# Kernel tuning notes

Measured on AMD Instinct MI355X. Metric: run time of the kernel, lower is better.

## Reference

```python
import jax, jax.numpy as jnp
import numpy as np

LAYERS = 2
N_NODE = 100000
EMB = 112
BATCH = 512
SEQ = 50
NNZ = 1600000


def setup_inputs() -> dict:
    key = jax.random.key(0)
    ks = jax.random.split(key, 12)
    embedding = jax.random.normal(ks[0], (N_NODE, EMB), jnp.float32) * 0.1
    adj_rows = jax.random.randint(ks[1], (NNZ,), 0, N_NODE, jnp.int32)
    adj_cols = jax.random.randint(ks[2], (NNZ,), 0, N_NODE, jnp.int32)
    adj_vals = jax.random.uniform(ks[3], (NNZ,), jnp.float32) * 0.05  # normalized-ish weights
    W_q = jax.random.normal(ks[4], (EMB, EMB), jnp.float32) * 0.1
    W_k = jax.random.normal(ks[5], (EMB, EMB), jnp.float32) * 0.1
    w_sess = jax.random.normal(ks[6], (LAYERS, EMB, EMB), jnp.float32) * 0.1
    D = jax.random.uniform(ks[7], (BATCH, BATCH), jnp.float32) * 0.01
    A = jax.random.uniform(ks[8], (BATCH, BATCH), jnp.float32)
    session_len = jax.random.randint(ks[9], (BATCH, 1), 1, SEQ + 1, jnp.int32)
    mask = (jnp.arange(SEQ)[None, :] < session_len).astype(jnp.float32)  # [B,L]
    raw_items = jax.random.randint(ks[10], (BATCH, SEQ), 1, N_NODE + 1, jnp.int32)
    session_item = jnp.where(mask > 0, raw_items, 0)  # 0 = padding row in cl_embed
    return {
        "embedding": embedding, "adj_vals": adj_vals, "W_q": W_q, "W_k": W_k,
        "w_sess": w_sess, "D": D, "A": A, "adj_rows": adj_rows,
        "adj_cols": adj_cols, "session_item": session_item,
        "session_len": session_len, "mask": mask,
    }


def reference(embedding, adj_vals, W_q, W_k, w_sess, D, A,
              adj_rows, adj_cols, session_item, session_len, mask):
    dt = embedding.dtype
    # ---- HyperConv: layers x sparse.mm, then mean over layer stack ----
    emb = embedding
    acc = embedding
    for _ in range(LAYERS):
        msg = adj_vals[:, None] * emb[adj_cols]              # [nnz, d]
        emb = jax.ops.segment_sum(msg, adj_rows, num_segments=N_NODE)
        acc = acc + emb
    item_emb = acc / (LAYERS + 1)                            # [N, d]

    # ---- SR_IEM sigmoid attention pooling ----
    d = jnp.asarray(EMB, dt)
    cl = jnp.concatenate([jnp.zeros((1, EMB), dt), item_emb], axis=0)
    seq = cl[session_item]                                   # [B,L,d]
    Q = jax.nn.sigmoid(jnp.einsum('bld,de->ble', seq, W_q))
    K = jax.nn.sigmoid(jnp.einsum('bld,de->ble', seq, W_k))
    C = jax.nn.sigmoid(jnp.einsum('ble,bme->blm', Q, K)) / jnp.sqrt(d)  # [B,L,L]
    C = C * (mask[:, :, None] * mask[:, None, :])
    C = C * (1.0 - jnp.eye(SEQ, dtype=dt))                   # remove diagonal
    alpha = jnp.sum(C, axis=2) / session_len.astype(dt)      # [B,L]
    # per-session softmax over the first session_len positions == masked softmax
    beta = jax.nn.softmax(jnp.where(mask > 0, alpha, -1e9), axis=1)
    seq_h = jnp.einsum('bl,bld->bd', beta, seq)              # [B,d]

    # ---- SessConv propagation over session graph ----
    DA = D @ A                                               # [B,B]
    s = seq_h
    acc2 = seq_h
    for i in range(LAYERS):
        s = s @ w_sess[i].T                                  # Linear, no bias
        s = DA @ s
        norm = jnp.maximum(jnp.linalg.norm(s, axis=-1, keepdims=True), 1e-12)
        acc2 = acc2 + s / norm                               # F.normalize(p=2)
    return acc2 / (LAYERS + 1)                               # [B,d]
```

## Files before the change

### kernel.cpp

```cpp
#include <hip/hip_runtime.h>

#define N_NODE 100000
#define EMB 112
#define EMBP 128
#define BATCH 512
#define SEQL 50
#define NNZ 1600000
#define NROWS (BATCH * SEQL)

#define BROWS 256
#define NBUCK ((N_NODE + BROWS - 1) / BROWS)
#define BUCK_CAP 4608
#define TILE_E 6250
#define P1_BLOCKS 256
#define NPREP1024 (N_NODE * 32 / 1024)

typedef _Float16 half2_t __attribute__((ext_vector_type(2)));

__device__ __forceinline__ float bf2f(unsigned short u) {
    return __uint_as_float((unsigned)u << 16);
}
__device__ __forceinline__ unsigned short f2bf(float f) {
    unsigned u = __float_as_uint(f);
    return (unsigned short)((u + 0x7FFF + ((u >> 16) & 1)) >> 16);
}
__device__ __forceinline__ float fdot2(half2_t a, half2_t b, float c) {
#if defined(__has_builtin)
#if __has_builtin(__builtin_amdgcn_fdot2)
    return __builtin_amdgcn_fdot2(a, b, c, false);
#else
    return c + (float)a[0] * (float)b[0] + (float)a[1] * (float)b[1];
#endif
#else
    return c + (float)a[0] * (float)b[0] + (float)a[1] * (float)b[1];
#endif
}

__global__ __launch_bounds__(1024) void prep_bin(
    const float* __restrict__ in, unsigned short* __restrict__ out,
    const int* __restrict__ rows, const int* __restrict__ cols,
    const float* __restrict__ vals,
    int* __restrict__ bcur, uint2* __restrict__ staged)
{
    __shared__ int hist[NBUCK];
    const int t = threadIdx.x;

    if (blockIdx.x >= P1_BLOCKS) {
        int i = (blockIdx.x - P1_BLOCKS) * 1024 + t;
        int r = i >> 5, c = i & 31;
        ushort4 o; o.x = 0; o.y = 0; o.z = 0; o.w = 0;
        if (c < 28) {
            float4 v = ((const float4*)in)[r * 28 + c];
            o.x = f2bf(v.x); o.y = f2bf(v.y); o.z = f2bf(v.z); o.w = f2bf(v.w);
        }
        ((ushort4*)out)[i] = o;
        return;
    }

    const int e0 = blockIdx.x * TILE_E;
    const int e1 = e0 + TILE_E;

    for (int i = t; i < NBUCK; i += 1024) hist[i] = 0;
    __syncthreads();
    for (int e = e0 + t; e < e1; e += 1024)
        atomicAdd(&hist[rows[e] >> 8], 1);
    __syncthreads();
    for (int i = t; i < NBUCK; i += 1024) {
        int c = hist[i];
        hist[i] = (c > 0) ? atomicAdd(&bcur[i], c) : 0;
    }
    __syncthreads();
    for (int e = e0 + t; e < e1; e += 1024) {
        int r = rows[e];
        int b = r >> 8;
        int k = atomicAdd(&hist[b], 1);
        uint2 s;
        s.x = ((unsigned)(r & 255) << 24) | (unsigned)cols[e];
        s.y = __float_as_uint(vals[e]);
        staged[(size_t)b * BUCK_CAP + k] = s;
    }
}

__global__ __launch_bounds__(1024) void bucket_csr_spmm(
    const uint2* __restrict__ staged, const int* __restrict__ bcur,
    const unsigned short* __restrict__ src, unsigned short* __restrict__ dst,
    int2* __restrict__ csr_cv, int* __restrict__ row_start,
    int* __restrict__ counts)
{
    __shared__ uint2 s_sorted[BUCK_CAP];
    __shared__ int cnt[BROWS];
    __shared__ int sc[BROWS];
    __shared__ int cur[BROWS];

    const int b = blockIdx.x;
    const int t = threadIdx.x;
    const int n = bcur[b];
    const size_t base = (size_t)b * BUCK_CAP;
    const int r0 = b << 8;

    if (t < BROWS) cnt[t] = 0;
    __syncthreads();
    for (int i = t; i < n; i += 1024)
        atomicAdd(&cnt[staged[base + i].x >> 24], 1);
    __syncthreads();

    if (t < BROWS) sc[t] = cnt[t];
    __syncthreads();
    for (int o = 1; o < BROWS; o <<= 1) {
        int v = 0;
        if (t < BROWS && t >= o) v = sc[t - o];
        __syncthreads();
        if (t < BROWS) sc[t] += v;
        __syncthreads();
    }
    if (t < BROWS) {
        int excl = sc[t] - cnt[t];
        cur[t] = excl;
        int row = r0 + t;
        if (row < N_NODE) {
            row_start[row] = (int)base + excl;
            counts[row] = cnt[t];
        }
    }
    __syncthreads();

    for (int i = t; i < n; i += 1024) {
        uint2 s = staged[base + i];
        int rl = s.x >> 24;
        int k = atomicAdd(&cur[rl], 1);
        uint2 e;
        e.x = s.x & 0x00FFFFFFu;
        e.y = s.y;
        s_sorted[k] = e;
    }
    __syncthreads();

    for (int i = t; i < n; i += 1024) {
        uint2 e = s_sorted[i];
        int2 cv; cv.x = (int)e.x; cv.y = (int)e.y;
        csr_cv[base + i] = cv;
    }

    const int wave = t >> 6;
    const int lane = t & 63;
    const int half = lane >> 5;
    const int hl = lane & 31;
    const int d0 = hl * 4;

    for (int it = 0; it < 8; ++it) {
        int rl = wave * 16 + it * 2 + half;
        int row = r0 + rl;
        bool valid = row < N_NODE;
        int n_r = valid ? cnt[rl] : 0;
        int beg = valid ? (sc[rl] - cnt[rl]) : 0;

        float a0 = 0.f, a1 = 0.f, a2 = 0.f, a3 = 0.f;
        int i = 0;
        for (; i + 8 <= n_r; i += 8) {
            #pragma unroll
            for (int j = 0; j < 8; ++j) {
                uint2 e = s_sorted[beg + i + j];
                float v = __uint_as_float(e.y);
                ushort4 u = *(const ushort4*)(src + (size_t)e.x * EMBP + d0);
                a0 += v * bf2f(u.x);
                a1 += v * bf2f(u.y);
                a2 += v * bf2f(u.z);
                a3 += v * bf2f(u.w);
            }
        }
        for (; i < n_r; ++i) {
            uint2 e = s_sorted[beg + i];
            float v = __uint_as_float(e.y);
            ushort4 u = *(const ushort4*)(src + (size_t)e.x * EMBP + d0);
            a0 += v * bf2f(u.x);
            a1 += v * bf2f(u.y);
            a2 += v * bf2f(u.z);
            a3 += v * bf2f(u.w);
        }
        if (valid) {
            ushort4 o;
            o.x = f2bf(a0); o.y = f2bf(a1); o.z = f2bf(a2); o.w = f2bf(a3);
            *(ushort4*)(dst + (size_t)row * EMBP + d0) = o;
        }
    }
}

__global__ __launch_bounds__(256) void gather_seq(
    const float* __restrict__ emb0,
    const unsigned short* __restrict__ e1b,
    const int2* __restrict__ csr_cv, const int* __restrict__ row_start,
    const int* __restrict__ counts,
    const int* __restrict__ items,
    float* __restrict__ seqg)
{
    const int t = threadIdx.x;
    const int hw = t >> 5;
    const int hl = t & 31;
    const int d0 = hl * 4;
    const int slot = blockIdx.x * 8 + hw;
    if (slot >= NROWS) return;

    float a0 = 0.f, a1 = 0.f, a2 = 0.f, a3 = 0.f;
    const int g = items[slot];
    if (g > 0) {
        const int r = g - 1;
        const int n = counts[r];
        const int beg = row_start[r];
        int i = 0;
        for (; i + 8 <= n; i += 8) {
            #pragma unroll
            for (int j = 0; j < 8; ++j) {
                int2 cv = csr_cv[beg + i + j];
                float v = __int_as_float(cv.y);
                ushort4 u = *(const ushort4*)(e1b + (size_t)cv.x * EMBP + d0);
                a0 += v * bf2f(u.x);
                a1 += v * bf2f(u.y);
                a2 += v * bf2f(u.z);
                a3 += v * bf2f(u.w);
            }
        }
        for (; i < n; ++i) {
            int2 cv = csr_cv[beg + i];
            float v = __int_as_float(cv.y);
            ushort4 u = *(const ushort4*)(e1b + (size_t)cv.x * EMBP + d0);
            a0 += v * bf2f(u.x);
            a1 += v * bf2f(u.y);
            a2 += v * bf2f(u.z);
            a3 += v * bf2f(u.w);
        }
        ushort4 u1 = *(const ushort4*)(e1b + (size_t)r * EMBP + d0);
        a0 += bf2f(u1.x); a1 += bf2f(u1.y); a2 += bf2f(u1.z); a3 += bf2f(u1.w);
        if (hl < 28) {
            float4 v0 = *(const float4*)(emb0 + (size_t)r * EMB + d0);
            a0 += v0.x; a1 += v0.y; a2 += v0.z; a3 += v0.w;
        }
        a0 *= (1.f / 3.f); a1 *= (1.f / 3.f);
        a2 *= (1.f / 3.f); a3 *= (1.f / 3.f);
    }
    if (hl < 28) {
        float4 w; w.x = a0; w.y = a1; w.z = a2; w.w = a3;
        *(float4*)(seqg + (size_t)slot * EMB + d0) = w;
    }
}

#define APAD 116
#define HPAD 120
struct AttnSmem {
    float s_seq[52][APAD];
    _Float16 sQ[SEQL][HPAD];
    _Float16 sK[SEQL][HPAD];
    float s_part[SEQL][4];
    float s_mask[SEQL];
    float s_beta[SEQL];
};
struct GemmSmem {
    float sD[32][33];
    float sA[32][33];
};
union AttnDaSmem { AttnSmem a; GemmSmem g; };

__global__ __launch_bounds__(256, 3) void attn_da(
    const float* __restrict__ seqg,
    const float* __restrict__ Wq, const float* __restrict__ Wk,
    const int* __restrict__ session_len, const float* __restrict__ mask,
    const float* __restrict__ D, const float* __restrict__ A,
    float* __restrict__ DA,
    float* __restrict__ seq_h, float* __restrict__ acc2)
{
    __shared__ AttnDaSmem sm;
    const int t = threadIdx.x;

    if (blockIdx.x >= BATCH) {
        const int bid = blockIdx.x - BATCH;
        const int i0 = (bid >> 4) * 32;
        const int j0 = (bid & 15) * 32;
        const int tx = t & 15;
        const int ty = t >> 4;
        float a00 = 0.f, a01 = 0.f, a10 = 0.f, a11 = 0.f;
        for (int k0 = 0; k0 < BATCH; k0 += 32) {
            for (int idx = t; idx < 1024; idx += 256) {
                int r = idx >> 5, c = idx & 31;
                sm.g.sD[r][c] = D[(i0 + r) * BATCH + k0 + c];
                sm.g.sA[r][c] = A[(k0 + r) * BATCH + j0 + c];
            }
            __syncthreads();
            #pragma unroll 8
            for (int kk = 0; kk < 32; ++kk) {
                float d0 = sm.g.sD[2 * ty][kk], d1 = sm.g.sD[2 * ty + 1][kk];
                float b0 = sm.g.sA[kk][2 * tx], b1 = sm.g.sA[kk][2 * tx + 1];
                a00 += d0 * b0; a01 += d0 * b1;
                a10 += d1 * b0; a11 += d1 * b1;
            }
            __syncthreads();
        }
        DA[(i0 + 2 * ty) * BATCH + j0 + 2 * tx] = a00;
        DA[(i0 + 2 * ty) * BATCH + j0 + 2 * tx + 1] = a01;
        DA[(i0 + 2 * ty + 1) * BATCH + j0 + 2 * tx] = a10;
        DA[(i0 + 2 * ty + 1) * BATCH + j0 + 2 * tx + 1] = a11;
        return;
    }

    const int b = blockIdx.x;
    const int slen_i = session_len[b];

    for (int u = t; u < SEQL * 28; u += 256) {
        int l = u / 28;
        int q = u - l * 28;
        *(float4*)&sm.a.s_seq[l][q * 4] =
            *(const float4*)(seqg + (size_t)(b * SEQL + l) * EMB + q * 4);
    }
    if (t < 2 * 28) {
        int l = SEQL + (t / 28);
        int q = t - (t / 28) * 28;
        float4 z; z.x = 0.f; z.y = 0.f; z.z = 0.f; z.w = 0.f;
        *(float4*)&sm.a.s_seq[l][q * 4] = z;
    }
    __syncthreads();

    const int rgmax = (slen_i + 3) >> 2;
    for (int u = t; u < rgmax * 28; u += 256) {
        const int rg = u / 28;
        const int e0 = (u - rg * 28) * 4;
        float accq[4][4] = {{0.f}}, acck[4][4] = {{0.f}};
        #pragma unroll 2
        for (int d4 = 0; d4 < 28; ++d4) {
            float sa[4][4];
            #pragma unroll
            for (int rr = 0; rr < 4; ++rr) {
                float4 v = *(const float4*)&sm.a.s_seq[rg * 4 + rr][d4 * 4];
                sa[rr][0] = v.x; sa[rr][1] = v.y; sa[rr][2] = v.z; sa[rr][3] = v.w;
            }
            #pragma unroll
            for (int j = 0; j < 4; ++j) {
                const int d = d4 * 4 + j;
                float4 wq = *(const float4*)&Wq[d * EMB + e0];
                float4 wk = *(const float4*)&Wk[d * EMB + e0];
                #pragma unroll
                for (int rr = 0; rr < 4; ++rr) {
                    float s = sa[rr][j];
                    accq[rr][0] += s * wq.x; accq[rr][1] += s * wq.y;
                    accq[rr][2] += s * wq.z; accq[rr][3] += s * wq.w;
                    acck[rr][0] += s * wk.x; acck[rr][1] += s * wk.y;
                    acck[rr][2] += s * wk.z; acck[rr][3] += s * wk.w;
                }
            }
        }
        #pragma unroll
        for (int rr = 0; rr < 4; ++rr) {
            int row = rg * 4 + rr;
            if (row < slen_i) {
                float q0 = 1.f / (1.f + __expf(-accq[rr][0]));
                float q1 = 1.f / (1.f + __expf(-accq[rr][1]));
                float q2 = 1.f / (1.f + __expf(-accq[rr][2]));
                float q3 = 1.f / (1.f + __expf(-accq[rr][3]));
                float k0 = 1.f / (1.f + __expf(-acck[rr][0]));
                float k1 = 1.f / (1.f + __expf(-acck[rr][1]));
                float k2 = 1.f / (1.f + __expf(-acck[rr][2]));
                float k3 = 1.f / (1.f + __expf(-acck[rr][3]));
                half2_t hq0 = {(_Float16)q0, (_Float16)q1};
                half2_t hq1 = {(_Float16)q2, (_Float16)q3};
                half2_t hk0 = {(_Float16)k0, (_Float16)k1};
                half2_t hk1 = {(_Float16)k2, (_Float16)k3};
                *(half2_t*)&sm.a.sQ[row][e0]     = hq0;
                *(half2_t*)&sm.a.sQ[row][e0 + 2] = hq1;
                *(half2_t*)&sm.a.sK[row][e0]     = hk0;
                *(half2_t*)&sm.a.sK[row][e0 + 2] = hk1;
            }
        }
    }
    __syncthreads();

    const float inv_sqrt_d = rsqrtf((float)EMB);
    if (t < 200) {
        const int l = t >> 2;
        const int m0 = t & 3;
        float partial = 0.f;
        if (l < slen_i) {
            const half2_t* qp = (const half2_t*)&sm.a.sQ[l][0];
            for (int m = m0; m < slen_i; m += 4) {
                if (m == l) continue;
                const half2_t* kp = (const half2_t*)&sm.a.sK[m][0];
                float d0 = 0.f, d1 = 0.f, d2 = 0.f, d3 = 0.f;
                #pragma unroll
                for (int d = 0; d < 56; d += 4) {
                    d0 = fdot2(qp[d],     kp[d],     d0);
                    d1 = fdot2(qp[d + 1], kp[d + 1], d1);
                    d2 = fdot2(qp[d + 2], kp[d + 2], d2);
                    d3 = fdot2(qp[d + 3], kp[d + 3], d3);
                }
                float dot = (d0 + d1) + (d2 + d3);
                partial += inv_sqrt_d / (1.f + __expf(-dot));
            }
        }
        sm.a.s_part[l][m0] = partial;
    }
    __syncthreads();

    if (t < 64) {
        float slen = (float)slen_i;
        float a = -1e30f;
        if (t < slen_i)
            a = (sm.a.s_part[t][0] + sm.a.s_part[t][1] +
                 sm.a.s_part[t][2] + sm.a.s_part[t][3]) / slen;
        float mx = a;
        for (int o = 32; o > 0; o >>= 1) mx = fmaxf(mx, __shfl_xor(mx, o));
        float ex = __expf(a - mx);
        float sm_ = ex;
        for (int o = 32; o > 0; o >>= 1) sm_ += __shfl_xor(sm_, o);
        if (t < SEQL) sm.a.s_beta[t] = ex / sm_;
    }
    __syncthreads();

    if (t < EMB) {
        float h = 0.f;
        for (int l = 0; l < slen_i; ++l) h += sm.a.s_beta[l] * sm.a.s_seq[l][t];
        seq_h[b * EMB + t] = h;
        acc2[b * EMB + t] = h;
    }
}

__global__ __launch_bounds__(128) void sess_fused(
    const float* __restrict__ DA, const float* __restrict__ s_in,
    const float* __restrict__ W,
    float* __restrict__ s_out, float* __restrict__ acc2,
    float* __restrict__ out, int is_last)
{
    __shared__ float da[BATCH];
    __shared__ float u[EMB];
    __shared__ float red[128];
    const int b = blockIdx.x;
    const int e = threadIdx.x;

    for (int k = e; k < BATCH; k += 128) da[k] = DA[b * BATCH + k];
    __syncthreads();

    float uu = 0.f;
    if (e < EMB) {
        #pragma unroll 8
        for (int k = 0; k < BATCH; ++k) uu += da[k] * s_in[k * EMB + e];
        u[e] = uu;
    }
    __syncthreads();

    float v = 0.f;
    if (e < EMB) {
        #pragma unroll 8
        for (int d = 0; d < EMB; ++d) v += u[d] * W[e * EMB + d];
    }
    red[e] = (e < EMB) ? v * v : 0.f;
    __syncthreads();
    for (int off = 64; off > 0; off >>= 1) {
        if (e < off) red[e] += red[e + off];
        __syncthreads();
    }
    float nrm = fmaxf(sqrtf(red[0]), 1e-12f);
    if (e < EMB) {
        float a = acc2[b * EMB + e] + v / nrm;
        acc2[b * EMB + e] = a;
        s_out[b * EMB + e] = v;
        if (is_last) out[b * EMB + e] = a * (1.f / 3.f);
    }
}

extern "C" void kernel_launch(void* const* d_in, const int* in_sizes, int n_in,
                              void* d_out, int out_size, void* d_ws, size_t ws_size,
                              hipStream_t stream)
{
    (void)in_sizes; (void)n_in; (void)out_size; (void)ws_size;

    const float* embedding    = (const float*)d_in[0];
    const float* adj_vals     = (const float*)d_in[1];
    const float* W_q          = (const float*)d_in[2];
    const float* W_k          = (const float*)d_in[3];
    const float* w_sess       = (const float*)d_in[4];
    const float* D            = (const float*)d_in[5];
    const float* A            = (const float*)d_in[6];
    const int*   adj_rows     = (const int*)d_in[7];
    const int*   adj_cols     = (const int*)d_in[8];
    const int*   session_item = (const int*)d_in[9];
    const int*   session_len  = (const int*)d_in[10];
    const float* mask         = (const float*)d_in[11];
    float* out = (float*)d_out;

    unsigned short* ebf0 = (unsigned short*)d_ws;
    unsigned short* ebf1 = ebf0 + (size_t)N_NODE * EMBP;
    float* DAb       = (float*)(ebf1 + (size_t)N_NODE * EMBP);
    float* seqh      = DAb  + (size_t)BATCH * BATCH;
    float* acc2      = seqh + (size_t)BATCH * EMB;
    float* sbuf      = acc2 + (size_t)BATCH * EMB;
    int*   counts    = (int*)(sbuf + (size_t)BATCH * EMB);
    int*   row_start = counts + N_NODE;
    int*   bcur      = row_start + N_NODE;
    int2*  csr_cv    = (int2*)(bcur + 2048);
    uint2* staged    = (uint2*)(csr_cv + (size_t)NBUCK * BUCK_CAP);
    float* seqg      = (float*)staged;

    hipMemsetAsync(bcur, 0, 2048 * sizeof(int), stream);

    prep_bin<<<P1_BLOCKS + NPREP1024, 1024, 0, stream>>>(
        embedding, ebf0, adj_rows, adj_cols, adj_vals, bcur, staged);

    bucket_csr_spmm<<<NBUCK, 1024, 0, stream>>>(staged, bcur, ebf0, ebf1,
                                                csr_cv, row_start, counts);

    gather_seq<<<NROWS / 8, 256, 0, stream>>>(embedding, ebf1, csr_cv,
                                              row_start, counts, session_item,
                                              seqg);

    attn_da<<<BATCH + 256, 256, 0, stream>>>(seqg, W_q, W_k, session_len, mask,
                                             D, A, DAb, seqh, acc2);

    sess_fused<<<BATCH, 128, 0, stream>>>(DAb, seqh, w_sess + 0 * EMB * EMB,
                                          sbuf, acc2, out, 0);
    sess_fused<<<BATCH, 128, 0, stream>>>(DAb, sbuf, w_sess + 1 * EMB * EMB,
                                          sbuf, acc2, out, 1);
}
```

Measured before the change: 319.0 us.

## Move DA GEMM into bucket SpMM kernel and fuse session layers cooperatively

The D@A product now runs as 64 extra blocks of 64x64 tiles inside the bucket SpMM launch instead of the attention kernel. This takes it off the attention stage's critical path and leaves attention blocks as pure pooling. The two session-propagation launches are merged into one cooperative kernel that uses a grid-wide sync between layers, saving a launch. In exchange, the 1024-thread GEMM blocks share the SpMM grid, and the cooperative launch requires all 512 blocks to be co-resident.

Measured after the change: 375.9 us. +17.8%, slower.

```diff
diff --git a/kernel.cpp b/kernel.cpp
--- a/kernel.cpp
+++ b/kernel.cpp
@@ -1,4 +1,7 @@
 #include <hip/hip_runtime.h>
+#include <hip/hip_cooperative_groups.h>
+
+namespace cg = cooperative_groups;
 
 #define N_NODE 100000
 #define EMB 112
@@ -14,6 +17,7 @@
 #define TILE_E 6250
 #define P1_BLOCKS 256
 #define NPREP1024 (N_NODE * 32 / 1024)
+#define NGEMM 64
 
 typedef _Float16 half2_t __attribute__((ext_vector_type(2)));
 
@@ -81,45 +85,89 @@
     }
 }
 
+struct SortSmem {
+    uint2 s_sorted[BUCK_CAP];
+    int cnt[BROWS];
+    int sc[BROWS];
+    int cur[BROWS];
+};
+struct Gemm64Smem {
+    float sD[64][33];
+    float sA[32][65];
+};
+union BuckSmem { SortSmem s; Gemm64Smem g; };
+
 __global__ __launch_bounds__(1024) void bucket_csr_spmm(
     const uint2* __restrict__ staged, const int* __restrict__ bcur,
     const unsigned short* __restrict__ src, unsigned short* __restrict__ dst,
     int2* __restrict__ csr_cv, int* __restrict__ row_start,
-    int* __restrict__ counts)
+    int* __restrict__ counts,
+    const float* __restrict__ D, const float* __restrict__ A,
+    float* __restrict__ DA)
 {
-    __shared__ uint2 s_sorted[BUCK_CAP];
-    __shared__ int cnt[BROWS];
-    __shared__ int sc[BROWS];
-    __shared__ int cur[BROWS];
+    __shared__ BuckSmem sm;
+    const int t = threadIdx.x;
+
+    if (blockIdx.x >= NBUCK) {
+        const int bid = blockIdx.x - NBUCK;
+        const int i0 = (bid >> 3) * 64;
+        const int j0 = (bid & 7) * 64;
+        const int tx = t & 31;
+        const int ty = t >> 5;
+        float a00 = 0.f, a01 = 0.f, a10 = 0.f, a11 = 0.f;
+        for (int k0 = 0; k0 < BATCH; k0 += 32) {
+            int idx = t;
+            #pragma unroll
+            for (int rpt = 0; rpt < 2; ++rpt, idx += 1024) {
+                int r = idx >> 5, c = idx & 31;
+                sm.g.sD[r][c] = D[(i0 + r) * BATCH + k0 + c];
+                int r2 = idx >> 6, c2 = idx & 63;
+                sm.g.sA[r2][c2] = A[(k0 + r2) * BATCH + j0 + c2];
+            }
+            __syncthreads();
+            #pragma unroll 8
+            for (int kk = 0; kk < 32; ++kk) {
+                float d0 = sm.g.sD[2 * ty][kk], d1 = sm.g.sD[2 * ty + 1][kk];
+                float b0 = sm.g.sA[kk][2 * tx], b1 = sm.g.sA[kk][2 * tx + 1];
+                a00 += d0 * b0; a01 += d0 * b1;
+                a10 += d1 * b0; a11 += d1 * b1;
+            }
+            __syncthreads();
+        }
+        DA[(i0 + 2 * ty) * BATCH + j0 + 2 * tx] = a00;
+        DA[(i0 + 2 * ty) * BATCH + j0 + 2 * tx + 1] = a01;
+        DA[(i0 + 2 * ty + 1) * BATCH + j0 + 2 * tx] = a10;
+        DA[(i0 + 2 * ty + 1) * BATCH + j0 + 2 * tx + 1] = a11;
+        return;
+    }
 
     const int b = blockIdx.x;
-    const int t = threadIdx.x;
     const int n = bcur[b];
     const size_t base = (size_t)b * BUCK_CAP;
     const int r0 = b << 8;
 
-    if (t < BROWS) cnt[t] = 0;
+    if (t < BROWS) sm.s.cnt[t] = 0;
     __syncthreads();
     for (int i = t; i < n; i += 1024)
-        atomicAdd(&cnt[staged[base + i].x >> 24], 1);
-    __syncthreads();
-
-    if (t < BROWS) sc[t] = cnt[t];
+        atomicAdd(&sm.s.cnt[staged[base + i].x >> 24], 1);
+    __syncthreads();
+
+    if (t < BROWS) sm.s.sc[t] = sm.s.cnt[t];
     __syncthreads();
     for (int o = 1; o < BROWS; o <<= 1) {
         int v = 0;
-        if (t < BROWS && t >= o) v = sc[t - o];
+        if (t < BROWS && t >= o) v = sm.s.sc[t - o];
         __syncthreads();
-        if (t < BROWS) sc[t] += v;
+        if (t < BROWS) sm.s.sc[t] += v;
         __syncthreads();
     }
     if (t < BROWS) {
-        int excl = sc[t] - cnt[t];
-        cur[t] = excl;
+        int excl = sm.s.sc[t] - sm.s.cnt[t];
+        sm.s.cur[t] = excl;
         int row = r0 + t;
         if (row < N_NODE) {
             row_start[row] = (int)base + excl;
-            counts[row] = cnt[t];
+            counts[row] = sm.s.cnt[t];
         }
     }
     __syncthreads();
@@ -127,16 +175,16 @@
     for (int i = t; i < n; i += 1024) {
         uint2 s = staged[base + i];
         int rl = s.x >> 24;
-        int k = atomicAdd(&cur[rl], 1);
+        int k = atomicAdd(&sm.s.cur[rl], 1);
         uint2 e;
         e.x = s.x & 0x00FFFFFFu;
         e.y = s.y;
-        s_sorted[k] = e;
+        sm.s.s_sorted[k] = e;
     }
     __syncthreads();
 
     for (int i = t; i < n; i += 1024) {
-        uint2 e = s_sorted[i];
+        uint2 e = sm.s.s_sorted[i];
         int2 cv; cv.x = (int)e.x; cv.y = (int)e.y;
         csr_cv[base + i] = cv;
     }
@@ -151,15 +199,15 @@
         int rl = wave * 16 + it * 2 + half;
         int row = r0 + rl;
         bool valid = row < N_NODE;
-        int n_r = valid ? cnt[rl] : 0;
-        int beg = valid ? (sc[rl] - cnt[rl]) : 0;
+        int n_r = valid ? sm.s.cnt[rl] : 0;
+        int beg = valid ? (sm.s.sc[rl] - sm.s.cnt[rl]) : 0;
 
         float a0 = 0.f, a1 = 0.f, a2 = 0.f, a3 = 0.f;
         int i = 0;
         for (; i + 8 <= n_r; i += 8) {
             #pragma unroll
             for (int j = 0; j < 8; ++j) {
-                uint2 e = s_sorted[beg + i + j];
+                uint2 e = sm.s.s_sorted[beg + i + j];
                 float v = __uint_as_float(e.y);
                 ushort4 u = *(const ushort4*)(src + (size_t)e.x * EMBP + d0);
                 a0 += v * bf2f(u.x);
@@ -169,7 +217,7 @@
             }
         }
         for (; i < n_r; ++i) {
-            uint2 e = s_sorted[beg + i];
+            uint2 e = sm.s.s_sorted[beg + i];
             float v = __uint_as_float(e.y);
             ushort4 u = *(const ushort4*)(src + (size_t)e.x * EMBP + d0);
             a0 += v * bf2f(u.x);
@@ -250,70 +298,31 @@
     _Float16 sQ[SEQL][HPAD];
     _Float16 sK[SEQL][HPAD];
     float s_part[SEQL][4];
-    float s_mask[SEQL];
     float s_beta[SEQL];
 };
-struct GemmSmem {
-    float sD[32][33];
-    float sA[32][33];
-};
-union AttnDaSmem { AttnSmem a; GemmSmem g; };
-
-__global__ __launch_bounds__(256, 3) void attn_da(
+
+__global__ __launch_bounds__(256, 3) void attn_pool(
     const float* __restrict__ seqg,
     const float* __restrict__ Wq, const float* __restrict__ Wk,
-    const int* __restrict__ session_len, const float* __restrict__ mask,
-    const float* __restrict__ D, const float* __restrict__ A,
-    float* __restrict__ DA,
+    const int* __restrict__ session_len,
     float* __restrict__ seq_h, float* __restrict__ acc2)
 {
-    __shared__ AttnDaSmem sm;
+    __shared__ AttnSmem sm;
     const int t = threadIdx.x;
-
-    if (blockIdx.x >= BATCH) {
-        const int bid = blockIdx.x - BATCH;
-        const int i0 = (bid >> 4) * 32;
-        const int j0 = (bid & 15) * 32;
-        const int tx = t & 15;
-        const int ty = t >> 4;
-        float a00 = 0.f, a01 = 0.f, a10 = 0.f, a11 = 0.f;
-        for (int k0 = 0; k0 < BATCH; k0 += 32) {
-            for (int idx = t; idx < 1024; idx += 256) {
-                int r = idx >> 5, c = idx & 31;
-                sm.g.sD[r][c] = D[(i0 + r) * BATCH + k0 + c];
-                sm.g.sA[r][c] = A[(k0 + r) * BATCH + j0 + c];
-            }
-            __syncthreads();
-            #pragma unroll 8
-            for (int kk = 0; kk < 32; ++kk) {
-                float d0 = sm.g.sD[2 * ty][kk], d1 = sm.g.sD[2 * ty + 1][kk];
-                float b0 = sm.g.sA[kk][2 * tx], b1 = sm.g.sA[kk][2 * tx + 1];
-                a00 += d0 * b0; a01 += d0 * b1;
-                a10 += d1 * b0; a11 += d1 * b1;
-            }
-            __syncthreads();
-        }
-        DA[(i0 + 2 * ty) * BATCH + j0 + 2 * tx] = a00;
-        DA[(i0 + 2 * ty) * BATCH + j0 + 2 * tx + 1] = a01;
-        DA[(i0 + 2 * ty + 1) * BATCH + j0 + 2 * tx] = a10;
-        DA[(i0 + 2 * ty + 1) * BATCH + j0 + 2 * tx + 1] = a11;
-        return;
-    }
-
     const int b = blockIdx.x;
     const int slen_i = session_len[b];
 
     for (int u = t; u < SEQL * 28; u += 256) {
         int l = u / 28;
         int q = u - l * 28;
-        *(float4*)&sm.a.s_seq[l][q * 4] =
+        *(float4*)&sm.s_seq[l][q * 4] =
             *(const float4*)(seqg + (size_t)(b * SEQL + l) * EMB + q * 4);
     }
     if (t < 2 * 28) {
         int l = SEQL + (t / 28);
         int q = t - (t / 28) * 28;
         float4 z; z.x = 0.f; z.y = 0.f; z.z = 0.f; z.w = 0.f;
-        *(float4*)&sm.a.s_seq[l][q * 4] = z;
+        *(float4*)&sm.s_seq[l][q * 4] = z;
     }
     __syncthreads();
 
@@ -327,7 +336,7 @@
             float sa[4][4];
             #pragma unroll
             for (int rr = 0; rr < 4; ++rr) {
-                float4 v = *(const float4*)&sm.a.s_seq[rg * 4 + rr][d4 * 4];
+                float4 v = *(const float4*)&sm.s_seq[rg * 4 + rr][d4 * 4];
                 sa[rr][0] = v.x; sa[rr][1] = v.y; sa[rr][2] = v.z; sa[rr][3] = v.w;
             }
             #pragma unroll
@@ -361,10 +370,10 @@
                 half2_t hq1 = {(_Float16)q2, (_Float16)q3};
                 half2_t hk0 = {(_Float16)k0, (_Float16)k1};
                 half2_t hk1 = {(_Float16)k2, (_Float16)k3};
-                *(half2_t*)&sm.a.sQ[row][e0]     = hq0;
-                *(half2_t*)&sm.a.sQ[row][e0 + 2] = hq1;
-                *(half2_t*)&sm.a.sK[row][e0]     = hk0;
-                *(half2_t*)&sm.a.sK[row][e0 + 2] = hk1;
+                *(half2_t*)&sm.sQ[row][e0]     = hq0;
+                *(half2_t*)&sm.sQ[row][e0 + 2] = hq1;
+                *(half2_t*)&sm.sK[row][e0]     = hk0;
+                *(half2_t*)&sm.sK[row][e0 + 2] = hk1;
             }
         }
     }
@@ -376,10 +385,10 @@
         const int m0 = t & 3;
         float partial = 0.f;
         if (l < slen_i) {
-            const half2_t* qp = (const half2_t*)&sm.a.sQ[l][0];
+            const half2_t* qp = (const half2_t*)&sm.sQ[l][0];
             for (int m = m0; m < slen_i; m += 4) {
                 if (m == l) continue;
-                const half2_t* kp = (const half2_t*)&sm.a.sK[m][0];
+                const half2_t* kp = (const half2_t*)&sm.sK[m][0];
                 float d0 = 0.f, d1 = 0.f, d2 = 0.f, d3 = 0.f;
                 #pragma unroll
                 for (int d = 0; d < 56; d += 4) {
@@ -392,7 +401,7 @@
                 partial += inv_sqrt_d / (1.f + __expf(-dot));
             }
         }
-        sm.a.s_part[l][m0] = partial;
+        sm.s_part[l][m0] = partial;
     }
     __syncthreads();
 
@@ -400,30 +409,30 @@
         float slen = (float)slen_i;
         float a = -1e30f;
         if (t < slen_i)
-            a = (sm.a.s_part[t][0] + sm.a.s_part[t][1] +
-                 sm.a.s_part[t][2] + sm.a.s_part[t][3]) / slen;
+            a = (sm.s_part[t][0] + sm.s_part[t][1] +
+                 sm.s_part[t][2] + sm.s_part[t][3]) / slen;
         float mx = a;
         for (int o = 32; o > 0; o >>= 1) mx = fmaxf(mx, __shfl_xor(mx, o));
         float ex = __expf(a - mx);
         float sm_ = ex;
         for (int o = 32; o > 0; o >>= 1) sm_ += __shfl_xor(sm_, o);
-        if (t < SEQL) sm.a.s_beta[t] = ex / sm_;
+        if (t < SEQL) sm.s_beta[t] = ex / sm_;
     }
     __syncthreads();
 
     if (t < EMB) {
         float h = 0.f;
-        for (int l = 0; l < slen_i; ++l) h += sm.a.s_beta[l] * sm.a.s_seq[l][t];
+        for (int l = 0; l < slen_i; ++l) h += sm.s_beta[l] * sm.s_seq[l][t];
         seq_h[b * EMB + t] = h;
         acc2[b * EMB + t] = h;
     }
 }
 
-__global__ __launch_bounds__(128) void sess_fused(
-    const float* __restrict__ DA, const float* __restrict__ s_in,
+__global__ __launch_bounds__(128) void sess_both(
+    const float* __restrict__ DA, const float* __restrict__ seqh,
     const float* __restrict__ W,
-    float* __restrict__ s_out, float* __restrict__ acc2,
-    float* __restrict__ out, int is_last)
+    float* __restrict__ sbuf, float* __restrict__ acc2,
+    float* __restrict__ out)
 {
     __shared__ float da[BATCH];
     __shared__ float u[EMB];
@@ -437,11 +446,10 @@
     float uu = 0.f;
     if (e < EMB) {
         #pragma unroll 8
-        for (int k = 0; k < BATCH; ++k) uu += da[k] * s_in[k * EMB + e];
+        for (int k = 0; k < BATCH; ++k) uu += da[k] * seqh[k * EMB + e];
         u[e] = uu;
     }
     __syncthreads();
-
     float v = 0.f;
     if (e < EMB) {
         #pragma unroll 8
@@ -455,10 +463,34 @@
     }
     float nrm = fmaxf(sqrtf(red[0]), 1e-12f);
     if (e < EMB) {
-        float a = acc2[b * EMB + e] + v / nrm;
-        acc2[b * EMB + e] = a;
-        s_out[b * EMB + e] = v;
-        if (is_last) out[b * EMB + e] = a * (1.f / 3.f);
+        acc2[b * EMB + e] = acc2[b * EMB + e] + v / nrm;
+        sbuf[b * EMB + e] = v;
+    }
+
+    cg::this_grid().sync();
+
+    float uu2 = 0.f;
+    if (e < EMB) {
+        #pragma unroll 8
+        for (int k = 0; k < BATCH; ++k) uu2 += da[k] * sbuf[k * EMB + e];
+        u[e] = uu2;
+    }
+    __syncthreads();
+    float v2 = 0.f;
+    if (e < EMB) {
+        #pragma unroll 8
+        for (int d = 0; d < EMB; ++d) v2 += u[d] * W[EMB * EMB + e * EMB + d];
+    }
+    red[e] = (e < EMB) ? v2 * v2 : 0.f;
+    __syncthreads();
+    for (int off = 64; off > 0; off >>= 1) {
+        if (e < off) red[e] += red[e + off];
+        __syncthreads();
+    }
+    float nrm2 = fmaxf(sqrtf(red[0]), 1e-12f);
+    if (e < EMB) {
+        float a = acc2[b * EMB + e] + v2 / nrm2;
+        out[b * EMB + e] = a * (1.f / 3.f);
     }
 }
 
@@ -479,7 +511,6 @@
     const int*   adj_cols     = (const int*)d_in[8];
     const int*   session_item = (const int*)d_in[9];
     const int*   session_len  = (const int*)d_in[10];
-    const float* mask         = (const float*)d_in[11];
     float* out = (float*)d_out;
 
     unsigned short* ebf0 = (unsigned short*)d_ws;
@@ -500,18 +531,18 @@
     prep_bin<<<P1_BLOCKS + NPREP1024, 1024, 0, stream>>>(
         embedding, ebf0, adj_rows, adj_cols, adj_vals, bcur, staged);
 
-    bucket_csr_spmm<<<NBUCK, 1024, 0, stream>>>(staged, bcur, ebf0, ebf1,
-                                                csr_cv, row_start, counts);
+    bucket_csr_spmm<<<NBUCK + NGEMM, 1024, 0, stream>>>(
+        staged, bcur, ebf0, ebf1, csr_cv, row_start, counts, D, A, DAb);
 
     gather_seq<<<NROWS / 8, 256, 0, stream>>>(embedding, ebf1, csr_cv,
                                               row_start, counts, session_item,
                                               seqg);
 
-    attn_da<<<BATCH + 256, 256, 0, stream>>>(seqg, W_q, W_k, session_len, mask,
-                                             D, A, DAb, seqh, acc2);
-
-    sess_fused<<<BATCH, 128, 0, stream>>>(DAb, seqh, w_sess + 0 * EMB * EMB,
-                                          sbuf, acc2, out, 0);
-    sess_fused<<<BATCH, 128, 0, stream>>>(DAb, sbuf, w_sess + 1 * EMB * EMB,
-                                          sbuf, acc2, out, 1);
-}
+    attn_pool<<<BATCH, 256, 0, stream>>>(seqg, W_q, W_k, session_len,
+                                         seqh, acc2);
+
+    void* args[] = { (void*)&DAb, (void*)&seqh, (void*)&w_sess,
+                     (void*)&sbuf, (void*)&acc2, (void*)&out };
+    hipLaunchCooperativeKernel((const void*)sess_both, dim3(BATCH), dim3(128),
+                               args, 0, stream);
+}
```
